# Kernel optimization log

Measured on AMD Instinct MI355X. Metric: run time of the kernel, lower is better.

Reference implementation:

```python
import jax, jax.numpy as jnp
import numpy as np

N_NODES = 50000
N_EDGES = 1600000
D_IN = 512
D_OUT = 512


def setup_inputs() -> dict:
    key = jax.random.key(0)
    k1, k2, k3, k4, k5 = jax.random.split(key, 5)
    inputs = jax.random.normal(k1, (N_NODES, D_IN), dtype=jnp.float32)
    # xavier_uniform for weight [D_IN, D_OUT]
    limit = float(np.sqrt(6.0 / (D_IN + D_OUT)))
    weight = jax.random.uniform(k2, (D_IN, D_OUT), dtype=jnp.float32, minval=-limit, maxval=limit)
    adj_rows = jnp.sort(jax.random.randint(k3, (N_EDGES,), 0, N_NODES, dtype=jnp.int32))
    adj_cols = jax.random.randint(k4, (N_EDGES,), 0, N_NODES, dtype=jnp.int32)
    adj_vals = jax.random.uniform(k5, (N_EDGES,), dtype=jnp.float32)
    return {"inputs": inputs, "weight": weight, "adj_rows": adj_rows,
            "adj_cols": adj_cols, "adj_vals": adj_vals}


def reference(inputs, weight, adj_rows, adj_cols, adj_vals):
    # dropout(p=0.0) is identity in this configuration
    support = inputs @ weight                      # [N, D_OUT] dense GEMM
    gathered = support[adj_cols] * adj_vals[:, None]   # [E, D_OUT]
    output = jax.ops.segment_sum(gathered, adj_rows, num_segments=N_NODES)  # spmm
    return output
```

## Files before the change

### kernel.cpp

```cpp
#include <hip/hip_runtime.h>
#include <hip/hip_bf16.h>

#define N_NODES 50000
#define N_EDGES 1600000
#define D 512

typedef __attribute__((ext_vector_type(8))) short short8;
typedef __attribute__((ext_vector_type(4))) float f32x4;
typedef __attribute__((ext_vector_type(2))) float f32x2;
typedef __attribute__((ext_vector_type(8))) unsigned short u16x8;

__device__ __forceinline__ void async_copy16(const void* g, void* l) {
    __builtin_amdgcn_global_load_lds(
        (const __attribute__((address_space(1))) unsigned int*)g,
        (__attribute__((address_space(3))) unsigned int*)l, 16, 0, 0);
}

__global__ __launch_bounds__(256) void wt_kernel(const float* __restrict__ W,
                                                 unsigned short* __restrict__ Wt) {
    int idx = blockIdx.x * 256 + threadIdx.x;
    int k = idx >> 9;
    int n = idx & 511;
    Wt[n * D + k] = __bfloat16_as_ushort(__float2bfloat16(W[k * D + n]));
}

__global__ __launch_bounds__(256) void rowptr_kernel(const int* __restrict__ rows,
                                                     int* __restrict__ row_start) {
    int r = blockIdx.x * 256 + threadIdx.x;
    if (r > N_NODES) return;
    int lo = 0, hi = N_EDGES;
    while (lo < hi) {
        int mid = (lo + hi) >> 1;
        if (rows[mid] < r) lo = mid + 1; else hi = mid;
    }
    row_start[r] = lo;
}

#define BM 128
#define BN 256
#define BK 32

__global__ __launch_bounds__(512, 2) void gemm_kernel(const float* __restrict__ X,
                                                      const unsigned short* __restrict__ Wt,
                                                      __hip_bfloat16* __restrict__ support) {
    __shared__ unsigned short As[2][BM * BK];
    __shared__ unsigned short Bs[2][BN * BK];

    const int t = threadIdx.x;
    const int lane = t & 63;
    const int w = t >> 6;
    const int wm = (w >> 2) * 64;
    const int wn = (w & 3) * 64;
    const int bid = blockIdx.x;
    const int m0 = (bid >> 1) * BM;
    const int n0 = (bid & 1) * BN;
    const int l15 = lane & 15;
    const int quad = lane >> 4;

    f32x4 acc[4][4];
#pragma unroll
    for (int i = 0; i < 4; ++i)
#pragma unroll
        for (int j = 0; j < 4; ++j) acc[i][j] = (f32x4)(0.0f);

    int arow = m0 + (t >> 2);
    if (arow > N_NODES - 1) arow = N_NODES - 1;
    const float* abase = X + (size_t)arow * D + (t & 3) * 8;
    const int awr = (t >> 2) * BK + (t & 3) * 8;


    {
        f32x4 a0 = *(const f32x4*)abase;
        f32x4 a1 = *(const f32x4*)(abase + 4);
#pragma unroll
        for (int c = 0; c < 2; ++c) {
            int cid = c * 512 + t;
            async_copy16(Wt + (size_t)(n0 + (cid >> 2)) * D + (cid & 3) * 8,
                         &Bs[0][cid * 8]);
        }
        u16x8 u;
#pragma unroll
        for (int k = 0; k < 4; ++k) {
            u[k]     = __bfloat16_as_ushort(__float2bfloat16(a0[k]));
            u[k + 4] = __bfloat16_as_ushort(__float2bfloat16(a1[k]));
        }
        *(u16x8*)(&As[0][awr]) = u;
    }
    __syncthreads();

    int cur = 0;
    for (int kt = 0; kt < D / BK; ++kt) {
        f32x4 a0n, a1n;
        const int nxt = cur ^ 1;
        if (kt < D / BK - 1) {
            const int k0n = (kt + 1) * BK;
            a0n = *(const f32x4*)(abase + k0n);
            a1n = *(const f32x4*)(abase + k0n + 4);
#pragma unroll
            for (int c = 0; c < 2; ++c) {
                int cid = c * 512 + t;
                async_copy16(Wt + (size_t)(n0 + (cid >> 2)) * D + k0n + (cid & 3) * 8,
                             &Bs[nxt][cid * 8]);
            }
        }

        short8 af[4], bf[4];
#pragma unroll
        for (int i = 0; i < 4; ++i) af[i] = *(const short8*)(&As[cur][(wm + i * 16 + l15) * BK + quad * 8]);
#pragma unroll
        for (int j = 0; j < 4; ++j) bf[j] = *(const short8*)(&Bs[cur][(wn + j * 16 + l15) * BK + quad * 8]);
#pragma unroll
        for (int i = 0; i < 4; ++i)
#pragma unroll
            for (int j = 0; j < 4; ++j)
                acc[i][j] = __builtin_amdgcn_mfma_f32_16x16x32_bf16(af[i], bf[j], acc[i][j], 0, 0, 0);

        if (kt < D / BK - 1) {
            u16x8 u;
#pragma unroll
            for (int k = 0; k < 4; ++k) {
                u[k]     = __bfloat16_as_ushort(__float2bfloat16(a0n[k]));
                u[k + 4] = __bfloat16_as_ushort(__float2bfloat16(a1n[k]));
            }
            *(u16x8*)(&As[nxt][awr]) = u;
        }
        __syncthreads();
        cur ^= 1;
    }

#pragma unroll
    for (int i = 0; i < 4; ++i) {
        int grow = m0 + wm + i * 16 + quad * 4;
#pragma unroll
        for (int j = 0; j < 4; ++j) {
            int gc = n0 + wn + j * 16 + l15;
#pragma unroll
            for (int rr = 0; rr < 4; ++rr) {
                int gr = grow + rr;
                if (gr < N_NODES)
                    support[(size_t)gr * D + gc] = __float2bfloat16(acc[i][j][rr]);
            }
        }
    }
}

__global__ __launch_bounds__(256) void spmm_kernel(const unsigned short* __restrict__ support,
                                                   const int* __restrict__ cols,
                                                   const float* __restrict__ vals,
                                                   const int* __restrict__ row_start,
                                                   float* __restrict__ out) {
    const int r = blockIdx.x;
    const int t = threadIdx.x;
    const int s = row_start[r];
    const int e = row_start[r + 1];
    const size_t co = 2 * t;

    float ax = 0.f, ay = 0.f;
    int i = s;
    for (; i + 8 <= e; i += 8) {
        int c[8]; float v[8]; unsigned int h[8];
#pragma unroll
        for (int k = 0; k < 8; ++k) { c[k] = cols[i + k]; v[k] = vals[i + k]; }
#pragma unroll
        for (int k = 0; k < 8; ++k)
            h[k] = *(const unsigned int*)(support + (size_t)c[k] * D + co);
#pragma unroll
        for (int k = 0; k < 8; ++k) {
            ax += v[k] * __uint_as_float(h[k] << 16);
            ay += v[k] * __uint_as_float(h[k] & 0xffff0000u);
        }
    }
    for (; i < e; ++i) {
        int c = cols[i];
        float v = vals[i];
        unsigned int h = *(const unsigned int*)(support + (size_t)c * D + co);
        ax += v * __uint_as_float(h << 16);
        ay += v * __uint_as_float(h & 0xffff0000u);
    }
    f32x2 o; o[0] = ax; o[1] = ay;
    __builtin_nontemporal_store(o, (f32x2*)(out + (size_t)r * D + co));
}

extern "C" void kernel_launch(void* const* d_in, const int* in_sizes, int n_in,
                              void* d_out, int out_size, void* d_ws, size_t ws_size,
                              hipStream_t stream) {
    (void)in_sizes; (void)n_in; (void)out_size; (void)ws_size;
    const float* X    = (const float*)d_in[0];
    const float* W    = (const float*)d_in[1];
    const int* rows   = (const int*)d_in[2];
    const int* cols   = (const int*)d_in[3];
    const float* vals = (const float*)d_in[4];
    float* out = (float*)d_out;

    unsigned short* support = (unsigned short*)d_ws;
    unsigned short* Wt      = support + (size_t)N_NODES * D;
    int* row_start          = (int*)(Wt + (size_t)D * D);

    wt_kernel<<<(D * D) / 256, 256, 0, stream>>>(W, Wt);
    rowptr_kernel<<<(N_NODES + 256) / 256, 256, 0, stream>>>(rows, row_start);

    const int mblocks = (N_NODES + BM - 1) / BM;
    gemm_kernel<<<mblocks * 2, 512, 0, stream>>>(X, Wt, (__hip_bfloat16*)support);

    spmm_kernel<<<N_NODES, 256, 0, stream>>>(support, cols, vals, row_start, out);
}
```

Before: 446.4 us.

## Split SpMM by column chunks with wave-per-row and edge-parallel lanes

Restructures the SpMM so each wave handles one row and a 32-column slice, with 4 lane groups processing different edges and a shuffle reduction at the end. A 2D grid over row groups and column chunks makes concurrently running blocks touch the same narrow column slice of support, aiming for much better cache locality on the random gathers. In exchange, each gather is only 64 bytes per row and the edge indices and values are re-read once per column chunk.

```diff
diff --git a/kernel.cpp b/kernel.cpp
--- a/kernel.cpp
+++ b/kernel.cpp
@@ -68,7 +68,6 @@
     const float* abase = X + (size_t)arow * D + (t & 3) * 8;
     const int awr = (t >> 2) * BK + (t & 3) * 8;
 
-
     {
         f32x4 a0 = *(const f32x4*)abase;
         f32x4 a1 = *(const f32x4*)(abase + 4);
@@ -149,36 +148,45 @@
                                                    const float* __restrict__ vals,
                                                    const int* __restrict__ row_start,
                                                    float* __restrict__ out) {
-    const int r = blockIdx.x;
     const int t = threadIdx.x;
+    const int lane = t & 63;
+    const int wave = t >> 6;
+    const int r = blockIdx.x * 4 + wave;
+    const int chunk = blockIdx.y;
+    const int eg = lane >> 4;
+    const int cp = lane & 15;
     const int s = row_start[r];
     const int e = row_start[r + 1];
-    const size_t co = 2 * t;
+    const size_t co = (size_t)chunk * 32 + cp * 2;
 
     float ax = 0.f, ay = 0.f;
     int i = s;
     for (; i + 8 <= e; i += 8) {
-        int c[8]; float v[8]; unsigned int h[8];
-#pragma unroll
-        for (int k = 0; k < 8; ++k) { c[k] = cols[i + k]; v[k] = vals[i + k]; }
-#pragma unroll
-        for (int k = 0; k < 8; ++k)
-            h[k] = *(const unsigned int*)(support + (size_t)c[k] * D + co);
-#pragma unroll
-        for (int k = 0; k < 8; ++k) {
-            ax += v[k] * __uint_as_float(h[k] << 16);
-            ay += v[k] * __uint_as_float(h[k] & 0xffff0000u);
-        }
-    }
-    for (; i < e; ++i) {
-        int c = cols[i];
-        float v = vals[i];
+        int i0 = i + eg, i1 = i + 4 + eg;
+        int c0 = cols[i0]; float v0 = vals[i0];
+        int c1 = cols[i1]; float v1 = vals[i1];
+        unsigned int h0 = *(const unsigned int*)(support + (size_t)c0 * D + co);
+        unsigned int h1 = *(const unsigned int*)(support + (size_t)c1 * D + co);
+        ax += v0 * __uint_as_float(h0 << 16);
+        ay += v0 * __uint_as_float(h0 & 0xffff0000u);
+        ax += v1 * __uint_as_float(h1 << 16);
+        ay += v1 * __uint_as_float(h1 & 0xffff0000u);
+    }
+    for (; i < e; i += 4) {
+        int idx = i + eg;
+        int cidx = idx < e ? idx : i;
+        float v = idx < e ? vals[idx] : 0.f;
+        int c = cols[cidx];
         unsigned int h = *(const unsigned int*)(support + (size_t)c * D + co);
         ax += v * __uint_as_float(h << 16);
         ay += v * __uint_as_float(h & 0xffff0000u);
     }
-    f32x2 o; o[0] = ax; o[1] = ay;
-    __builtin_nontemporal_store(o, (f32x2*)(out + (size_t)r * D + co));
+    ax += __shfl_xor(ax, 16); ax += __shfl_xor(ax, 32);
+    ay += __shfl_xor(ay, 16); ay += __shfl_xor(ay, 32);
+    if (lane < 16) {
+        f32x2 o; o[0] = ax; o[1] = ay;
+        __builtin_nontemporal_store(o, (f32x2*)(out + (size_t)r * D + co));
+    }
 }
 
 extern "C" void kernel_launch(void* const* d_in, const int* in_sizes, int n_in,
@@ -202,5 +210,6 @@
     const int mblocks = (N_NODES + BM - 1) / BM;
     gemm_kernel<<<mblocks * 2, 512, 0, stream>>>(X, Wt, (__hip_bfloat16*)support);
 
-    spmm_kernel<<<N_NODES, 256, 0, stream>>>(support, cols, vals, row_start, out);
-}
+    dim3 sg(N_NODES / 4, D / 32);
+    spmm_kernel<<<sg, 256, 0, stream>>>(support, cols, vals, row_start, out);
+}
```

After: 674.5 us. 1.51x slower.

## Swizzle GEMM LDS tiles and replace syncthreads with manual waitcnt barriers

Applied to the files above, without the earlier changes.

Applies an XOR swizzle to the LDS layout of both the A and B tiles so MFMA fragment reads avoid bank conflicts. It also replaces the end-of-iteration __syncthreads with explicit vmcnt/lgkmcnt waits and a raw s_barrier at the top of each iteration, so the prefetch loads for the next tile can stay in flight across the barrier. The loop is unrolled by 2. The hand-written waitcnt counts must match the number of outstanding loads exactly, otherwise the kernel reads LDS before the data has landed.

```diff
diff --git a/kernel.cpp b/kernel.cpp
--- a/kernel.cpp
+++ b/kernel.cpp
@@ -39,6 +39,10 @@
 #define BM 128
 #define BN 256
 #define BK 32
+
+__device__ __forceinline__ int swz(int rc) {
+    return (rc ^ (rc >> 2)) & 3;
+}
 
 __global__ __launch_bounds__(512, 2) void gemm_kernel(const float* __restrict__ X,
                                                       const unsigned short* __restrict__ Wt,
@@ -63,20 +67,33 @@
 #pragma unroll
         for (int j = 0; j < 4; ++j) acc[i][j] = (f32x4)(0.0f);
 
-    int arow = m0 + (t >> 2);
+    const int arow_l = t >> 2;
+    int arow = m0 + arow_l;
     if (arow > N_NODES - 1) arow = N_NODES - 1;
     const float* abase = X + (size_t)arow * D + (t & 3) * 8;
-    const int awr = (t >> 2) * BK + (t & 3) * 8;
-
+    const int awr = (arow_l * 4 + ((t & 3) ^ swz(arow_l))) * 8;
+
+    int aoff[4], boff[4];
+#pragma unroll
+    for (int i = 0; i < 4; ++i) {
+        const int row = wm + i * 16 + l15;
+        aoff[i] = (row * 4 + (quad ^ swz(row))) * 8;
+    }
+#pragma unroll
+    for (int j = 0; j < 4; ++j) {
+        const int n = wn + j * 16 + l15;
+        boff[j] = (n * 4 + (quad ^ swz(n))) * 8;
+    }
 
     {
         f32x4 a0 = *(const f32x4*)abase;
         f32x4 a1 = *(const f32x4*)(abase + 4);
 #pragma unroll
         for (int c = 0; c < 2; ++c) {
-            int cid = c * 512 + t;
-            async_copy16(Wt + (size_t)(n0 + (cid >> 2)) * D + (cid & 3) * 8,
-                         &Bs[0][cid * 8]);
+            const int cid = c * 512 + t;
+            const int n = cid >> 2;
+            const int kcs = (cid & 3) ^ swz(n);
+            async_copy16(Wt + (size_t)(n0 + n) * D + kcs * 8, &Bs[0][cid * 8]);
         }
         u16x8 u;
 #pragma unroll
@@ -86,29 +103,40 @@
         }
         *(u16x8*)(&As[0][awr]) = u;
     }
-    __syncthreads();
 
     int cur = 0;
+#pragma unroll 2
     for (int kt = 0; kt < D / BK; ++kt) {
+        const int nxt = cur ^ 1;
+        const int k0n = (kt + 1) * BK;
         f32x4 a0n, a1n;
-        const int nxt = cur ^ 1;
         if (kt < D / BK - 1) {
-            const int k0n = (kt + 1) * BK;
             a0n = *(const f32x4*)(abase + k0n);
             a1n = *(const f32x4*)(abase + k0n + 4);
+            asm volatile("s_waitcnt vmcnt(2)" ::: "memory");
+        } else {
+            asm volatile("s_waitcnt vmcnt(0)" ::: "memory");
+        }
+        asm volatile("s_waitcnt lgkmcnt(0)" ::: "memory");
+        __builtin_amdgcn_sched_barrier(0);
+        __builtin_amdgcn_s_barrier();
+        __builtin_amdgcn_sched_barrier(0);
+
+        if (kt < D / BK - 1) {
 #pragma unroll
             for (int c = 0; c < 2; ++c) {
-                int cid = c * 512 + t;
-                async_copy16(Wt + (size_t)(n0 + (cid >> 2)) * D + k0n + (cid & 3) * 8,
-                             &Bs[nxt][cid * 8]);
+                const int cid = c * 512 + t;
+                const int n = cid >> 2;
+                const int kcs = (cid & 3) ^ swz(n);
+                async_copy16(Wt + (size_t)(n0 + n) * D + k0n + kcs * 8, &Bs[nxt][cid * 8]);
             }
         }
 
         short8 af[4], bf[4];
 #pragma unroll
-        for (int i = 0; i < 4; ++i) af[i] = *(const short8*)(&As[cur][(wm + i * 16 + l15) * BK + quad * 8]);
-#pragma unroll
-        for (int j = 0; j < 4; ++j) bf[j] = *(const short8*)(&Bs[cur][(wn + j * 16 + l15) * BK + quad * 8]);
+        for (int i = 0; i < 4; ++i) af[i] = *(const short8*)(&As[cur][aoff[i]]);
+#pragma unroll
+        for (int j = 0; j < 4; ++j) bf[j] = *(const short8*)(&Bs[cur][boff[j]]);
 #pragma unroll
         for (int i = 0; i < 4; ++i)
 #pragma unroll
@@ -124,7 +152,6 @@
             }
             *(u16x8*)(&As[nxt][awr]) = u;
         }
-        __syncthreads();
         cur ^= 1;
     }
 
```

Measured after the change: 439.2 us. No clear change (-1.6%).
